# Kernel optimization log

Hardware: AMD Instinct MI355X
Metric: run time of the kernel (lower is better)

Reference implementation:

```python
import jax, jax.numpy as jnp
import numpy as np

N_NODES = 50000
N_EDGES = 1600000
D_IN = 128
D_OUT = 128


def setup_inputs() -> dict:
    key = jax.random.key(0)
    k1, k2, k3, k4, k5 = jax.random.split(key, 5)
    x = jax.random.normal(k1, (N_NODES, D_IN), dtype=jnp.float32)
    edge_index = jax.random.randint(k2, (2, N_EDGES), 0, N_NODES, dtype=jnp.int64)
    s = 1.0 / np.sqrt(D_IN)
    W_l = jax.random.normal(k3, (D_OUT, D_IN), dtype=jnp.float32) * s
    b_l = jax.random.normal(k4, (D_OUT,), dtype=jnp.float32) * s
    W_r = jax.random.normal(k5, (D_OUT, D_IN), dtype=jnp.float32) * s
    return {"x": x, "edge_index": edge_index, "W_l": W_l, "b_l": b_l, "W_r": W_r}


def reference(x, edge_index, W_l, b_l, W_r):
    src, dst = edge_index[0], edge_index[1]
    # mean aggregation of neighbor (source) features at destination nodes
    agg = jax.ops.segment_sum(x[src], dst, num_segments=N_NODES)  # [N, D_in]
    cnt = jax.ops.segment_sum(jnp.ones((src.shape[0],), dtype=x.dtype), dst,
                              num_segments=N_NODES)
    mean = agg / jnp.maximum(cnt, 1.0)[:, None]
    # SAGEConv: lin_l(mean_neighbors) + lin_r(x_root); bias only on lin_l
    out = mean @ W_l.T + b_l + x @ W_r.T
    # last=False, act=relu, dropout inactive (p=0.0 / eval mode)
    return jax.nn.relu(out)
```

## Files before the change

### kernel.cpp

```cpp
#include <hip/hip_runtime.h>
#include <hip/hip_bf16.h>

#define NN 50000
#define NE 1600000
#define D  128
#define NB   500
#define NPB  100
#define RCAP 4224
#define NBB  512
#define ECH  3125
#define CASTB 1024
#define FRONTG (NBB + CASTB + 8)
#define NGRP 7

typedef unsigned int u32;
typedef unsigned long long u64;
typedef unsigned short u16;
typedef __attribute__((ext_vector_type(8))) short short8;
typedef __attribute__((ext_vector_type(4))) float f32x4;
typedef __attribute__((ext_vector_type(2))) float f32x2;

#define GCUR_OFF 0
#define REG_OFF  4096
#define XF8_OFF  8452096
#define XB_OFF   14852224
#define WB_OFF   27652224

__device__ __forceinline__ u32 pack2(float a, float b) {
    u32 ua = __float_as_uint(a), ub = __float_as_uint(b);
    ua = (ua + 0x7FFFu + ((ua >> 16) & 1u)) >> 16;
    ub = (ub + 0x7FFFu + ((ub >> 16) & 1u)) >> 16;
    return ua | (ub << 16);
}

__global__ __launch_bounds__(512) void k_front(const int* __restrict__ ei,
                                               const float* __restrict__ x,
                                               const float* __restrict__ Wl,
                                               const float* __restrict__ Wr,
                                               u32* __restrict__ gcur,
                                               u32* __restrict__ region,
                                               uint2* __restrict__ xf8,
                                               uint4* __restrict__ xb,
                                               uint4* __restrict__ Wb,
                                               u32* __restrict__ xzrow) {
    __shared__ u32 eL[ECH + 6];
    __shared__ u32 srt[ECH + 6];
    __shared__ u32 lh[512], sc[512], gb[512], lc[512];
    __shared__ u32 ps[256];

    const int bid = blockIdx.x;
    const int t = threadIdx.x;

    if (bid >= NBB + CASTB) {
        const int s = (bid - NBB - CASTB) * 512 + t;
        const int mat = s >> 11;
        const int j   = (s >> 4) & 127;
        const int k8  = (s & 15) * 8;
        const float* src = (mat ? Wr : Wl) + (size_t)j * 128 + k8;
        const float4 a = reinterpret_cast<const float4*>(src)[0];
        const float4 b = reinterpret_cast<const float4*>(src)[1];
        uint4 o;
        o.x = pack2(a.x, a.y); o.y = pack2(a.z, a.w);
        o.z = pack2(b.x, b.y); o.w = pack2(b.z, b.w);
        Wb[s] = o;
        if (s < 32) xzrow[s] = 0u;
        return;
    }

    if (bid >= NBB) {
        const int total = NN * D / 8;
        for (int i = (bid - NBB) * 512 + t; i < total; i += CASTB * 512) {
            const float4 a = reinterpret_cast<const float4*>(x)[2 * i];
            const float4 b = reinterpret_cast<const float4*>(x)[2 * i + 1];
            uint2 o8;
            o8.x = (u32)__builtin_amdgcn_cvt_pk_fp8_f32(a.z, a.w,
                     __builtin_amdgcn_cvt_pk_fp8_f32(a.x, a.y, 0, false), true);
            o8.y = (u32)__builtin_amdgcn_cvt_pk_fp8_f32(b.z, b.w,
                     __builtin_amdgcn_cvt_pk_fp8_f32(b.x, b.y, 0, false), true);
            xf8[i] = o8;
            uint4 ob;
            ob.x = pack2(a.x, a.y); ob.y = pack2(a.z, a.w);
            ob.z = pack2(b.x, b.y); ob.w = pack2(b.z, b.w);
            xb[i] = ob;
        }
        return;
    }

    const int lane = t & 63;
    const u64 zmask = __ballot((u32)ei[2 * lane + 1] == 0u);
    const bool is64 = (zmask == ~0ull);

    const int e0 = bid * ECH;

    lh[t] = 0u; lc[t] = 0u;
    __syncthreads();

    for (int i = t; i < ECH; i += 512) {
        const int e = e0 + i;
        int src, dst;
        if (is64) { src = ei[2 * (size_t)e]; dst = ei[2 * (size_t)(NE + e)]; }
        else      { src = ei[e];             dst = ei[NE + e]; }
        const u32 b2 = (u32)dst / NPB;
        const u32 dl = (u32)dst - b2 * NPB;
        eL[i] = (b2 << 23) | (dl << 16) | (u32)src;
        atomicAdd(&lh[b2], 1u);
    }
    __syncthreads();

    u32 a0 = 0u, a1 = 0u;
    if (t < 256) { a0 = lh[2 * t]; a1 = lh[2 * t + 1]; ps[t] = a0 + a1; }
    __syncthreads();
    for (int ofs = 1; ofs < 256; ofs <<= 1) {
        u32 v = 0u;
        if (t < 256 && t >= ofs) v = ps[t - ofs];
        __syncthreads();
        if (t < 256) ps[t] += v;
        __syncthreads();
    }
    if (t < 256) {
        const u32 base = ps[t] - (a0 + a1);
        sc[2 * t]     = base + a0;
        sc[2 * t + 1] = base + a0 + a1;
        if (a0) gb[2 * t]     = atomicAdd(&gcur[2 * t],     a0);
        if (a1) gb[2 * t + 1] = atomicAdd(&gcur[2 * t + 1], a1);
    }
    __syncthreads();

    for (int i = t; i < ECH; i += 512) {
        const u32 e = eL[i];
        const u32 b2 = e >> 23;
        const u32 lp = atomicAdd(&lc[b2], 1u);
        srt[(sc[b2] - lh[b2]) + lp] = e;
    }
    __syncthreads();

    for (int i = t; i < ECH; i += 512) {
        const u32 e    = srt[i];
        const u32 b2   = e >> 23;
        const u32 run0 = sc[b2] - lh[b2];
        const u32 pos  = gb[b2] + ((u32)i - run0);
        if (pos < RCAP) region[(size_t)b2 * RCAP + pos] = e;
    }
}

#define GLOAD(J) \
    const int  i##J = i + 2 * J + half; \
    const u32 ev##J = srt[i##J]; \
    const u32 sr##J = (i##J < s1) ? (ev##J & 0xFFFFu) : (u32)NN; \
    const u32 wv##J = xf8[(size_t)sr##J * 32 + q];

#define GACC(J) { \
    const f32x2 lo = __builtin_amdgcn_cvt_pk_f32_fp8((int)wv##J, false); \
    const f32x2 hi = __builtin_amdgcn_cvt_pk_f32_fp8((int)wv##J, true); \
    a01 += lo; a23 += hi; }

__global__ __launch_bounds__(1024, 8) void k_aggemm(const u32* __restrict__ xf8,
                                                    const u32* __restrict__ region,
                                                    const u32* __restrict__ gcur,
                                                    const uint4* __restrict__ xb,
                                                    const uint4* __restrict__ Wb,
                                                    const float* __restrict__ bl,
                                                    float* __restrict__ out) {
    __shared__ u32 srt[RCAP + 8];
    __shared__ u32 hist[128], segs[128], cur[128];
    __shared__ u16 As[16 * 256];
    __shared__ float part[2][16][128];

    const int t = threadIdx.x;
    const int b = blockIdx.x;

    if (t < 128) { hist[t] = 0u; cur[t] = 0u; }
    __syncthreads();

    u32 cnt = gcur[b];
    if (cnt > RCAP) cnt = RCAP;
    const u32* reg = region + (size_t)b * RCAP;

    for (int i = t; i < (int)cnt; i += 1024)
        atomicAdd(&hist[(reg[i] >> 16) & 0x7Fu], 1u);
    __syncthreads();

    if (t < 128) segs[t] = hist[t];
    __syncthreads();
    for (int ofs = 1; ofs < 128; ofs <<= 1) {
        u32 v = 0u;
        if (t < 128 && t >= ofs) v = segs[t - ofs];
        __syncthreads();
        if (t < 128) segs[t] += v;
        __syncthreads();
    }

    for (int i = t; i < (int)cnt; i += 1024) {
        const u32 e = reg[i];
        const u32 dl = (e >> 16) & 0x7Fu;
        const u32 p = (segs[dl] - hist[dl]) + atomicAdd(&cur[dl], 1u);
        srt[p] = e;
    }
    if (t < 8) srt[cnt + t] = (u32)NN;
    __syncthreads();

    const int w    = t >> 6;
    const int lane = t & 63;
    const int half = lane >> 5;
    const u32 q    = (u32)(lane & 31);
    const int m16  = lane & 15;
    const int kg   = lane >> 4;
    const int tc   = w & 7;
    const int kh   = w >> 3;
    const int row0 = b * NPB;

    const char* wbb = reinterpret_cast<const char*>(Wb) + kh * 32768
                    + (size_t)(tc * 16 + m16) * 256 + kg * 16;
    const short8 wf0 = *reinterpret_cast<const short8*>(wbb);
    const short8 wf1 = *reinterpret_cast<const short8*>(wbb + 64);
    const short8 wf2 = *reinterpret_cast<const short8*>(wbb + 128);
    const short8 wf3 = *reinterpret_cast<const short8*>(wbb + 192);
    const float bias = bl[tc * 16 + m16];

    const int sm   = t >> 4;
    const int slot = t & 15;
    const u32 byteX = ((u32)(sm * 512 + (128 + slot * 8) * 2)) ^ ((u32)(sm & 7) << 4);

    for (int g = 0; g < NGRP; ++g) {
        if (t < 256) {
            const int grow = g * 16 + sm;
            uint4 ox = {0u, 0u, 0u, 0u};
            if (grow < NPB) ox = xb[(size_t)(row0 + grow) * 16 + slot];
            *reinterpret_cast<uint4*>(reinterpret_cast<char*>(As) + byteX) = ox;
        }

        const int r = g * 16 + w;
        if (r < NPB) {
            const int deg = (int)hist[r];
            const int s1  = (int)segs[r];
            const int s0  = s1 - deg;

            f32x2 a01 = {0.f, 0.f}, a23 = {0.f, 0.f};
            for (int i = s0; i < s1; i += 8) {
                GLOAD(0) GLOAD(1) GLOAD(2) GLOAD(3)
                GACC(0) GACC(1) GACC(2) GACC(3)
            }

            const float r0 = a01.x + __shfl_xor(a01.x, 32);
            const float r1 = a01.y + __shfl_xor(a01.y, 32);
            const float r2 = a23.x + __shfl_xor(a23.x, 32);
            const float r3 = a23.y + __shfl_xor(a23.y, 32);

            if (lane < 32) {
                const float inv = deg ? 1.0f / (float)deg : 0.0f;
                uint2 o;
                o.x = pack2(r0 * inv, r1 * inv);
                o.y = pack2(r2 * inv, r3 * inv);
                const u32 byteM = ((u32)(w * 512 + q * 8)) ^ ((u32)(w & 7) << 4);
                *reinterpret_cast<uint2*>(reinterpret_cast<char*>(As) + byteM) = o;
            }
        }
        __syncthreads();

        f32x4 acc = {0.f, 0.f, 0.f, 0.f};
        {
            const int kbase = kh * 128;
            const u32 ab0 = ((u32)(m16 * 512 + (kbase +  0 + kg * 8) * 2)) ^ ((u32)(m16 & 7) << 4);
            const u32 ab1 = ((u32)(m16 * 512 + (kbase + 32 + kg * 8) * 2)) ^ ((u32)(m16 & 7) << 4);
            const u32 ab2 = ((u32)(m16 * 512 + (kbase + 64 + kg * 8) * 2)) ^ ((u32)(m16 & 7) << 4);
            const u32 ab3 = ((u32)(m16 * 512 + (kbase + 96 + kg * 8) * 2)) ^ ((u32)(m16 & 7) << 4);
            const short8 af0 = *reinterpret_cast<const short8*>(reinterpret_cast<const char*>(As) + ab0);
            const short8 af1 = *reinterpret_cast<const short8*>(reinterpret_cast<const char*>(As) + ab1);
            const short8 af2 = *reinterpret_cast<const short8*>(reinterpret_cast<const char*>(As) + ab2);
            const short8 af3 = *reinterpret_cast<const short8*>(reinterpret_cast<const char*>(As) + ab3);
            acc = __builtin_amdgcn_mfma_f32_16x16x32_bf16(af0, wf0, acc, 0, 0, 0);
            acc = __builtin_amdgcn_mfma_f32_16x16x32_bf16(af1, wf1, acc, 0, 0, 0);
            acc = __builtin_amdgcn_mfma_f32_16x16x32_bf16(af2, wf2, acc, 0, 0, 0);
            acc = __builtin_amdgcn_mfma_f32_16x16x32_bf16(af3, wf3, acc, 0, 0, 0);
        }

        if (kh == 1) {
            #pragma unroll
            for (int i = 0; i < 4; i++)
                part[g & 1][kg * 4 + i][tc * 16 + m16] = acc[i];
        }
        __syncthreads();

        if (kh == 0) {
            #pragma unroll
            for (int i = 0; i < 4; i++) {
                const int grow = g * 16 + kg * 4 + i;
                if (grow < NPB) {
                    const float s = acc[i] + part[g & 1][kg * 4 + i][tc * 16 + m16] + bias;
                    out[(size_t)(row0 + grow) * D + tc * 16 + m16] = fmaxf(s, 0.f);
                }
            }
        }
    }
}

extern "C" void kernel_launch(void* const* d_in, const int* in_sizes, int n_in,
                              void* d_out, int out_size, void* d_ws, size_t ws_size,
                              hipStream_t stream) {
    const float* x  = (const float*)d_in[0];
    const int*   ei = (const int*)  d_in[1];
    const float* Wl = (const float*)d_in[2];
    const float* bl = (const float*)d_in[3];
    const float* Wr = (const float*)d_in[4];

    char* ws = (char*)d_ws;
    u32*   gcur   = (u32*)(ws + GCUR_OFF);
    u32*   region = (u32*)(ws + REG_OFF);
    u32*   xf8    = (u32*)(ws + XF8_OFF);
    uint4* xb     = (uint4*)(ws + XB_OFF);
    uint4* Wb     = (uint4*)(ws + WB_OFF);
    float* out    = (float*)d_out;

    hipMemsetAsync(ws, 0, 4096, stream);
    k_front <<<FRONTG, 512, 0, stream>>>(ei, x, Wl, Wr, gcur, region,
                                         (uint2*)xf8, xb, Wb, xf8 + (size_t)NN * 32);
    k_aggemm<<<NB, 1024, 0, stream>>>(xf8, region, gcur, xb, Wb, bl, out);
}
```

Measured before the change: 84.67 us.

## Hoist neighbor aggregation out of GEMM loop and drop front-kernel local sort

The aggregation of all 100 node means per block now runs in one pass into a shared buffer before the GEMM loop, instead of being interleaved with per-group barriers. The x-operand MFMA fragments are loaded straight from global memory rather than staged through shared memory. The partials buffer gets a padded stride, and the front kernel scatters edges into regions directly using the local atomic offset, skipping an intermediate shared-memory sort pass. This cuts syncthreads and LDS traffic, at the cost of more shared memory per block (lower occupancy risk) and less coalesced global writes to the region.

```diff
diff --git a/kernel.cpp b/kernel.cpp
--- a/kernel.cpp
+++ b/kernel.cpp
@@ -12,6 +12,7 @@
 #define CASTB 1024
 #define FRONTG (NBB + CASTB + 8)
 #define NGRP 7
+#define PSTR 132
 
 typedef unsigned int u32;
 typedef unsigned long long u64;
@@ -44,7 +45,6 @@
                                                uint4* __restrict__ Wb,
                                                u32* __restrict__ xzrow) {
     __shared__ u32 eL[ECH + 6];
-    __shared__ u32 srt[ECH + 6];
     __shared__ u32 lh[512], sc[512], gb[512], lc[512];
     __shared__ u32 ps[256];
 
@@ -127,18 +127,10 @@
     __syncthreads();
 
     for (int i = t; i < ECH; i += 512) {
-        const u32 e = eL[i];
+        const u32 e  = eL[i];
         const u32 b2 = e >> 23;
         const u32 lp = atomicAdd(&lc[b2], 1u);
-        srt[(sc[b2] - lh[b2]) + lp] = e;
-    }
-    __syncthreads();
-
-    for (int i = t; i < ECH; i += 512) {
-        const u32 e    = srt[i];
-        const u32 b2   = e >> 23;
-        const u32 run0 = sc[b2] - lh[b2];
-        const u32 pos  = gb[b2] + ((u32)i - run0);
+        const u32 pos = gb[b2] + lp;
         if (pos < RCAP) region[(size_t)b2 * RCAP + pos] = e;
     }
 }
@@ -163,8 +155,8 @@
                                                     float* __restrict__ out) {
     __shared__ u32 srt[RCAP + 8];
     __shared__ u32 hist[128], segs[128], cur[128];
-    __shared__ u16 As[16 * 256];
-    __shared__ float part[2][16][128];
+    __shared__ u16 mbuf[NPB * 128];
+    __shared__ float part[2][16][PSTR];
 
     const int t = threadIdx.x;
     const int b = blockIdx.x;
@@ -209,6 +201,33 @@
     const int kh   = w >> 3;
     const int row0 = b * NPB;
 
+    for (int r = w; r < NPB; r += 16) {
+        const int deg = (int)hist[r];
+        const int s1  = (int)segs[r];
+        const int s0  = s1 - deg;
+
+        f32x2 a01 = {0.f, 0.f}, a23 = {0.f, 0.f};
+        for (int i = s0; i < s1; i += 8) {
+            GLOAD(0) GLOAD(1) GLOAD(2) GLOAD(3)
+            GACC(0) GACC(1) GACC(2) GACC(3)
+        }
+
+        const float r0 = a01.x + __shfl_xor(a01.x, 32);
+        const float r1 = a01.y + __shfl_xor(a01.y, 32);
+        const float r2 = a23.x + __shfl_xor(a23.x, 32);
+        const float r3 = a23.y + __shfl_xor(a23.y, 32);
+
+        if (lane < 32) {
+            const float inv = deg ? 1.0f / (float)deg : 0.0f;
+            uint2 o;
+            o.x = pack2(r0 * inv, r1 * inv);
+            o.y = pack2(r2 * inv, r3 * inv);
+            const u32 byteM = ((u32)(r * 256 + q * 8)) ^ ((u32)(r & 7) << 4);
+            *reinterpret_cast<uint2*>(reinterpret_cast<char*>(mbuf) + byteM) = o;
+        }
+    }
+    __syncthreads();
+
     const char* wbb = reinterpret_cast<const char*>(Wb) + kh * 32768
                     + (size_t)(tc * 16 + m16) * 256 + kg * 16;
     const short8 wf0 = *reinterpret_cast<const short8*>(wbb);
@@ -217,64 +236,32 @@
     const short8 wf3 = *reinterpret_cast<const short8*>(wbb + 192);
     const float bias = bl[tc * 16 + m16];
 
-    const int sm   = t >> 4;
-    const int slot = t & 15;
-    const u32 byteX = ((u32)(sm * 512 + (128 + slot * 8) * 2)) ^ ((u32)(sm & 7) << 4);
-
     for (int g = 0; g < NGRP; ++g) {
-        if (t < 256) {
-            const int grow = g * 16 + sm;
-            uint4 ox = {0u, 0u, 0u, 0u};
-            if (grow < NPB) ox = xb[(size_t)(row0 + grow) * 16 + slot];
-            *reinterpret_cast<uint4*>(reinterpret_cast<char*>(As) + byteX) = ox;
-        }
-
-        const int r = g * 16 + w;
-        if (r < NPB) {
-            const int deg = (int)hist[r];
-            const int s1  = (int)segs[r];
-            const int s0  = s1 - deg;
-
-            f32x2 a01 = {0.f, 0.f}, a23 = {0.f, 0.f};
-            for (int i = s0; i < s1; i += 8) {
-                GLOAD(0) GLOAD(1) GLOAD(2) GLOAD(3)
-                GACC(0) GACC(1) GACC(2) GACC(3)
-            }
-
-            const float r0 = a01.x + __shfl_xor(a01.x, 32);
-            const float r1 = a01.y + __shfl_xor(a01.y, 32);
-            const float r2 = a23.x + __shfl_xor(a23.x, 32);
-            const float r3 = a23.y + __shfl_xor(a23.y, 32);
-
-            if (lane < 32) {
-                const float inv = deg ? 1.0f / (float)deg : 0.0f;
-                uint2 o;
-                o.x = pack2(r0 * inv, r1 * inv);
-                o.y = pack2(r2 * inv, r3 * inv);
-                const u32 byteM = ((u32)(w * 512 + q * 8)) ^ ((u32)(w & 7) << 4);
-                *reinterpret_cast<uint2*>(reinterpret_cast<char*>(As) + byteM) = o;
-            }
-        }
-        __syncthreads();
+        const int grow = g * 16 + m16;
+        const int rowc = (grow < NPB) ? grow : (NPB - 1);
 
         f32x4 acc = {0.f, 0.f, 0.f, 0.f};
-        {
-            const int kbase = kh * 128;
-            const u32 ab0 = ((u32)(m16 * 512 + (kbase +  0 + kg * 8) * 2)) ^ ((u32)(m16 & 7) << 4);
-            const u32 ab1 = ((u32)(m16 * 512 + (kbase + 32 + kg * 8) * 2)) ^ ((u32)(m16 & 7) << 4);
-            const u32 ab2 = ((u32)(m16 * 512 + (kbase + 64 + kg * 8) * 2)) ^ ((u32)(m16 & 7) << 4);
-            const u32 ab3 = ((u32)(m16 * 512 + (kbase + 96 + kg * 8) * 2)) ^ ((u32)(m16 & 7) << 4);
-            const short8 af0 = *reinterpret_cast<const short8*>(reinterpret_cast<const char*>(As) + ab0);
-            const short8 af1 = *reinterpret_cast<const short8*>(reinterpret_cast<const char*>(As) + ab1);
-            const short8 af2 = *reinterpret_cast<const short8*>(reinterpret_cast<const char*>(As) + ab2);
-            const short8 af3 = *reinterpret_cast<const short8*>(reinterpret_cast<const char*>(As) + ab3);
+        if (kh == 0) {
+            const u32 rb = (u32)(rowc * 256) ;
+            const u32 sw = ((u32)(rowc & 7) << 4);
+            const short8 af0 = *reinterpret_cast<const short8*>(reinterpret_cast<const char*>(mbuf) + ((rb + (  0 + kg * 8) * 2) ^ sw));
+            const short8 af1 = *reinterpret_cast<const short8*>(reinterpret_cast<const char*>(mbuf) + ((rb + ( 32 + kg * 8) * 2) ^ sw));
+            const short8 af2 = *reinterpret_cast<const short8*>(reinterpret_cast<const char*>(mbuf) + ((rb + ( 64 + kg * 8) * 2) ^ sw));
+            const short8 af3 = *reinterpret_cast<const short8*>(reinterpret_cast<const char*>(mbuf) + ((rb + ( 96 + kg * 8) * 2) ^ sw));
             acc = __builtin_amdgcn_mfma_f32_16x16x32_bf16(af0, wf0, acc, 0, 0, 0);
             acc = __builtin_amdgcn_mfma_f32_16x16x32_bf16(af1, wf1, acc, 0, 0, 0);
             acc = __builtin_amdgcn_mfma_f32_16x16x32_bf16(af2, wf2, acc, 0, 0, 0);
             acc = __builtin_amdgcn_mfma_f32_16x16x32_bf16(af3, wf3, acc, 0, 0, 0);
-        }
-
-        if (kh == 1) {
+        } else {
+            const uint4* xrow = xb + (size_t)(row0 + rowc) * 16 + kg;
+            const short8 af0 = *reinterpret_cast<const short8*>(xrow);
+            const short8 af1 = *reinterpret_cast<const short8*>(xrow + 4);
+            const short8 af2 = *reinterpret_cast<const short8*>(xrow + 8);
+            const short8 af3 = *reinterpret_cast<const short8*>(xrow + 12);
+            acc = __builtin_amdgcn_mfma_f32_16x16x32_bf16(af0, wf0, acc, 0, 0, 0);
+            acc = __builtin_amdgcn_mfma_f32_16x16x32_bf16(af1, wf1, acc, 0, 0, 0);
+            acc = __builtin_amdgcn_mfma_f32_16x16x32_bf16(af2, wf2, acc, 0, 0, 0);
+            acc = __builtin_amdgcn_mfma_f32_16x16x32_bf16(af3, wf3, acc, 0, 0, 0);
             #pragma unroll
             for (int i = 0; i < 4; i++)
                 part[g & 1][kg * 4 + i][tc * 16 + m16] = acc[i];
@@ -284,10 +271,10 @@
         if (kh == 0) {
             #pragma unroll
             for (int i = 0; i < 4; i++) {
-                const int grow = g * 16 + kg * 4 + i;
-                if (grow < NPB) {
+                const int gr = g * 16 + kg * 4 + i;
+                if (gr < NPB) {
                     const float s = acc[i] + part[g & 1][kg * 4 + i][tc * 16 + m16] + bias;
-                    out[(size_t)(row0 + grow) * D + tc * 16 + m16] = fmaxf(s, 0.f);
+                    out[(size_t)(row0 + gr) * D + tc * 16 + m16] = fmaxf(s, 0.f);
                 }
             }
         }
```

Result: slower. 96.37 us (+13.8%).
